# Kernel optimization log

Hardware: AMD Instinct MI355X
Metric: run time of the kernel (lower is better)

Reference implementation:

```python
import jax, jax.numpy as jnp
import numpy as np

MAX_REL = 14
HEADS = 12
HEAD_DIM = 64
SCALE = HEAD_DIM ** -0.5


def _rel_indices(length):
    # Replicates ElasticRelativePosition2D index construction (static, numpy).
    L = length - 1
    s = int(L ** 0.5)
    r = np.arange(L)
    dv = r[None, :] // s - r[:, None] // s
    dh = r[None, :] % s - r[:, None] % s
    iv = np.clip(dv, -MAX_REL, MAX_REL) + MAX_REL + 1
    ih = np.clip(dh, -MAX_REL, MAX_REL) + MAX_REL + 1
    # pad top row and left col with index 0 (the CLS slot)
    iv = np.pad(iv, ((1, 0), (1, 0)), constant_values=0)
    ih = np.pad(ih, ((1, 0), (1, 0)), constant_values=0)
    return jnp.asarray(iv, dtype=jnp.int32), jnp.asarray(ih, dtype=jnp.int32)


def _rel_emb(table_v, table_h, length):
    iv, ih = _rel_indices(length)
    return table_v[iv] + table_h[ih]  # [length, length, 64]


def setup_inputs() -> dict:
    key = jax.random.key(0)
    ks = jax.random.split(key, 16)
    B, L, D = 32, 577, 768
    T = 2 * MAX_REL + 2  # 30
    std = 0.02
    inp = {
        "q": jax.random.normal(ks[0], (B, L, D), jnp.float32),
        "k": jax.random.normal(ks[1], (B, L, D), jnp.float32),
        "v": jax.random.normal(ks[2], (B, L, D), jnp.float32),
        "Wq": jax.random.normal(ks[3], (D, HEADS * HEAD_DIM), jnp.float32) * std,
        "bq": jnp.zeros((HEADS * HEAD_DIM,), jnp.float32),
        "Wk": jax.random.normal(ks[4], (D, HEADS * HEAD_DIM), jnp.float32) * std,
        "bk": jnp.zeros((HEADS * HEAD_DIM,), jnp.float32),
        "Wv": jax.random.normal(ks[5], (D, HEADS * HEAD_DIM), jnp.float32) * std,
        "bv": jnp.zeros((HEADS * HEAD_DIM,), jnp.float32),
        "Wp": jax.random.normal(ks[6], (HEADS * HEAD_DIM, D), jnp.float32) * std,
        "bp": jnp.zeros((D,), jnp.float32),
        "tab_vk": jax.random.normal(ks[7], (T, HEAD_DIM), jnp.float32) * std,
        "tab_hk": jax.random.normal(ks[8], (T, HEAD_DIM), jnp.float32) * std,
        "tab_vv": jax.random.normal(ks[9], (T, HEAD_DIM), jnp.float32) * std,
        "tab_hv": jax.random.normal(ks[10], (T, HEAD_DIM), jnp.float32) * std,
    }
    return inp


def reference(q, k, v, Wq, bq, Wk, bk, Wv, bv, Wp, bp, tab_vk, tab_hk, tab_vv, tab_hv):
    B, L, D = q.shape
    residual = q
    qh = (q @ Wq + bq).reshape(B, L, HEADS, HEAD_DIM).transpose(0, 2, 1, 3)  # [B,H,L,d]
    kh = (k @ Wk + bk).reshape(B, L, HEADS, HEAD_DIM).transpose(0, 2, 1, 3)
    vh = (v @ Wv + bv).reshape(B, L, HEADS, HEAD_DIM).transpose(0, 2, 1, 3)

    attn = jnp.einsum("bhid,bhjd->bhij", qh, kh) * SCALE
    r_p_k = _rel_emb(tab_vk, tab_hk, L)  # [L,L,d]
    attn = attn + jnp.einsum("bhid,ijd->bhij", qh, r_p_k)  # bias NOT scaled (as in source)
    attn = jax.nn.softmax(attn, axis=-1)

    out = jnp.einsum("bhij,bhjd->bhid", attn, vh)
    r_p_v = _rel_emb(tab_vv, tab_hv, L)
    out = out + jnp.einsum("bhij,ijd->bhid", attn, r_p_v)
    out = out.transpose(0, 2, 1, 3).reshape(B, L, HEADS * HEAD_DIM)

    out = out @ Wp + bp
    return out + residual
```

## Files before the change

kernel.cpp:

```cpp
#include <hip/hip_runtime.h>
#include <cstdint>


typedef unsigned short u16;
typedef unsigned int   u32;
typedef __attribute__((ext_vector_type(8))) __bf16 bf16x8;
typedef __attribute__((ext_vector_type(4))) float  f32x4;

#define B_   32
#define L_   577
#define D_   768
#define H_   12
#define HD_  64
#define LP_  640
#define M_   (B_*L_)
#define SCALE_ 0.125f

__device__ __forceinline__ float b2f(u16 u){ u32 x = ((u32)u) << 16; float f; __builtin_memcpy(&f,&x,4); return f; }
__device__ __forceinline__ u16 f2b(float f){ u32 x; __builtin_memcpy(&x,&f,4); u32 r = (x + 0x7FFFu + ((x>>16)&1u)) >> 16; return (u16)r; }

__device__ __forceinline__ f32x4 mfma_bf16(bf16x8 a, bf16x8 b, f32x4 c){
  return __builtin_amdgcn_mfma_f32_16x16x32_bf16(a, b, c, 0, 0, 0);
}

__device__ __forceinline__ void async16(const void* g, void* l){
  __builtin_amdgcn_global_load_lds(
    (const __attribute__((address_space(1))) void*)g,
    (__attribute__((address_space(3))) void*)l,
    16, 0, 0);
}

__device__ __forceinline__ void lds_fence(){
  asm volatile("s_waitcnt lgkmcnt(0)" ::: "memory");
}

__global__ __launch_bounds__(256) void ind_setup(u16* __restrict__ ind)
{
  int jt = blockIdx.x;
  int t  = threadIdx.x;
  int nt = t >> 6, lane = t & 63;
  int qq = lane >> 4, cc = lane & 15;
  int n = nt*16 + cc;
  u16 vals[8];
  #pragma unroll
  for (int idx = 0; idx < 8; ++idx){
    int j = jt*32 + qq*8 + idx;
    int bv, bhh;
    if (j == 0){ bv = 24; bhh = 24; }
    else { int jj = j-1; bv = jj/24; if (bv > 23) bv = 23; bhh = jj - (jj/24)*24; }
    bool one = (n < 25) ? (bv == n) : ((n < 50) ? (bhh == n-25) : false);
    vals[idx] = one ? (u16)0x3F80 : (u16)0;
  }
  *(uint4*)&ind[(size_t)((jt*4 + nt)*64 + lane)*8] = *(uint4*)vals;
}

__global__ __launch_bounds__(256) void tab_setup(
    const float* __restrict__ tvk, const float* __restrict__ thk,
    const float* __restrict__ tvv, const float* __restrict__ thv,
    u16* __restrict__ tabK, u16* __restrict__ tabVT)
{
  int i = blockIdx.x*256 + threadIdx.x;
  if (i >= 64*64) return;
  int r = i >> 6, col = i & 63;
  float kv = 0.f;
  if (r < 30)      kv = tvk[r*HD_ + col];
  else if (r < 60) kv = thk[(r-30)*HD_ + col];
  tabK[i] = f2b(kv);
  float vv = 0.f;
  if (col < 30)      vv = tvv[col*HD_ + r];
  else if (col < 60) vv = thv[(col-30)*HD_ + r];
  tabVT[i] = f2b(vv);
}

__global__ __launch_bounds__(256) void cvt3_bf16(
    const float* __restrict__ q, const float* __restrict__ k, const float* __restrict__ v,
    u16* __restrict__ dq, u16* __restrict__ dk, u16* __restrict__ dv)
{
  int z = blockIdx.y;
  const float* s = (z==0)?q:(z==1)?k:v;
  u16*         d = (z==0)?dq:(z==1)?dk:dv;
  int i = blockIdx.x*256 + threadIdx.x;
  if (i >= (M_*D_)/8) return;
  const float4* s4 = (const float4*)s;
  float4 a = s4[2*i], b = s4[2*i+1];
  uint4 o;
  o.x = (u32)f2b(a.x) | ((u32)f2b(a.y)<<16);
  o.y = (u32)f2b(a.z) | ((u32)f2b(a.w)<<16);
  o.z = (u32)f2b(b.x) | ((u32)f2b(b.y)<<16);
  o.w = (u32)f2b(b.z) | ((u32)f2b(b.w)<<16);
  ((uint4*)d)[i] = o;
}

__global__ __launch_bounds__(256) void transpose768(
    const float* __restrict__ W0, const float* __restrict__ W1,
    const float* __restrict__ W2, const float* __restrict__ W3,
    u16* __restrict__ T0, u16* __restrict__ T1, u16* __restrict__ T2, u16* __restrict__ T3)
{
  __shared__ float t[32][33];
  int z = blockIdx.z;
  const float* W = (z==0)?W0:(z==1)?W1:(z==2)?W2:W3;
  u16*         T = (z==0)?T0:(z==1)?T1:(z==2)?T2:T3;
  int kb = blockIdx.x*32, nb = blockIdx.y*32;
  int tx = threadIdx.x & 31, ty = threadIdx.x >> 5;
  #pragma unroll
  for (int r=0;r<32;r+=8) t[ty+r][tx] = W[(size_t)(kb+ty+r)*768 + nb+tx];
  __syncthreads();
  #pragma unroll
  for (int r=0;r<32;r+=8) T[(size_t)(nb+ty+r)*768 + kb+tx] = f2b(t[tx][ty+r]);
}

__global__ __launch_bounds__(256) void vtr_kernel(
    const u16* __restrict__ vh, u16* __restrict__ vhT)
{
  __shared__ __align__(16) u16 t[64][72];
  int ll0 = blockIdx.x * 64;
  size_t bhs = (size_t)(blockIdx.z*H_ + blockIdx.y) * LP_ * HD_;
  const u16* src = vh + bhs;
  u16* dst = vhT + bhs;
  int tid = threadIdx.x;
  #pragma unroll
  for (int it=0; it<2; ++it){
    int idx = it*256 + tid;
    int row = idx >> 3, ch = (idx & 7)*8;
    uint4 d4; d4.x=0u; d4.y=0u; d4.z=0u; d4.w=0u;
    if (ll0 + row < L_) d4 = *(const uint4*)(src + (size_t)(ll0+row)*HD_ + ch);
    *(uint4*)&t[row][ch] = d4;
  }
  __syncthreads();
  #pragma unroll
  for (int it=0; it<2; ++it){
    int idx = it*256 + tid;
    int dd = idx >> 3, l8 = (idx & 7)*8;
    u16 vals[8];
    #pragma unroll
    for (int e=0;e<8;++e) vals[e] = t[l8+e][dd];
    *(uint4*)(dst + (size_t)dd*LP_ + ll0 + l8) = *(uint4*)vals;
  }
}

__global__ __launch_bounds__(256) void gemm_kernel(
    const u16* __restrict__ A, const u16* __restrict__ BT,
    const float* __restrict__ bias, const float* __restrict__ resid,
    void* __restrict__ Dstv, int mode)
{
  __shared__ __align__(16) u16 AsL[128*32];
  __shared__ __align__(16) u16 BsL[128*32];
  const int blk = blockIdx.x;
  const int x = blk & 7, g = blk >> 3;
  const int n0 = (g % 6) * 128;
  const int m_idx = (g / 6) * 8 + x;
  if (m_idx >= 145) return;
  const int m0 = m_idx * 128;

  const int tid = threadIdx.x;
  const int w = tid>>6, lane = tid&63, q = lane>>4, c = lane&15;
  const int wr = w>>1, wc = w&1;

  f32x4 acc[4][4];
  #pragma unroll
  for (int ai=0;ai<4;++ai)
    #pragma unroll
    for (int bi=0;bi<4;++bi){ f32x4 z = {0.f,0.f,0.f,0.f}; acc[ai][bi] = z; }

  for (int k0 = 0; k0 < 768; k0 += 32){
    __syncthreads();
    #pragma unroll
    for (int t2 = 0; t2 < 2; ++t2){
      int idx = t2*256 + tid;
      int row = idx >> 2, ch = idx & 3;
      int mrow = m0 + row; if (mrow > M_-1) mrow = M_-1;
      const u16* srcA;
      if (mode < 3) srcA = A + (size_t)mrow*768 + k0 + ch*8;
      else {
        int bb = mrow / L_, ll = mrow - bb*L_;
        int hh = k0 >> 6, dd = (k0 & 63) + ch*8;
        srcA = A + (((size_t)(bb*H_ + hh)*LP_ + ll) << 6) + dd;
      }
      async16(srcA, (char*)AsL + (size_t)(t2*256 + w*64)*16);
      async16(BT + (size_t)(n0 + row)*768 + k0 + ch*8, (char*)BsL + (size_t)(t2*256 + w*64)*16);
    }
    __syncthreads();

    bf16x8 af[4], bf2[4];
    #pragma unroll
    for (int ai=0;ai<4;++ai) af[ai]  = *(const bf16x8*)&AsL[(wr*64 + ai*16 + c)*32 + q*8];
    #pragma unroll
    for (int bi=0;bi<4;++bi) bf2[bi] = *(const bf16x8*)&BsL[(wc*64 + bi*16 + c)*32 + q*8];
    #pragma unroll
    for (int ai=0;ai<4;++ai)
      #pragma unroll
      for (int bi=0;bi<4;++bi)
        acc[ai][bi] = mfma_bf16(af[ai], bf2[bi], acc[ai][bi]);
  }

  #pragma unroll
  for (int ai=0;ai<4;++ai){
    #pragma unroll
    for (int r2=0;r2<4;++r2){
      int mrow = m0 + wr*64 + ai*16 + q*4 + r2;
      if (mrow >= M_) continue;
      int bb = mrow / L_;
      int ll = mrow - bb*L_;
      #pragma unroll
      for (int bi=0;bi<4;++bi){
        int col = n0 + wc*64 + bi*16 + c;
        float vv = acc[ai][bi][r2] + bias[col];
        if (mode < 3){
          int hh = col >> 6, dd = col & 63;
          ((u16*)Dstv)[(((size_t)(bb*H_ + hh)*LP_ + ll) << 6) + dd] = f2b(vv);
        } else {
          size_t o2 = (size_t)mrow*768 + col;
          ((float*)Dstv)[o2] = vv + resid[o2];
        }
      }
    }
  }
}

__global__ __launch_bounds__(256) void attn_kernel(
    const u16* __restrict__ qh, const u16* __restrict__ kh, const u16* __restrict__ vhT,
    const u16* __restrict__ tabK, const u16* __restrict__ tabVT,
    const u16* __restrict__ ind,
    u16* __restrict__ oh)
{
  __shared__ __align__(16) char sb[4*6272];
  const int tid = threadIdx.x;
  const int w = tid>>6, lane = tid&63, q = lane>>4, c = lane&15;
  char* wb = sb + w*6272;
  float* gvh   = (float*)wb;
  u16*   pvhb  = (u16*)wb;
  u16*   Ps_w  = (u16*)(wb + 3328);
  u16*   bias_t= (u16*)(wb + 4608);

  const int id = blockIdx.x;
  const int lin = (id & 7)*480 + (id >> 3);
  const int qt = lin % 10;
  const int hb = lin / 10;
  const int h = hb % 12, b = hb / 12;

  const int i0 = qt * 64;
  const size_t bh = (size_t)(b*H_ + h) * LP_ * HD_;
  const u16* qh_b = qh + bh;
  const u16* kh_b = kh + bh;
  const u16* vT_b = vhT + bh;

  bf16x8 aq0 = *(const bf16x8*)(qh_b + (size_t)(i0 + w*16 + c)*HD_ + q*8);
  bf16x8 aq1 = *(const bf16x8*)(qh_b + (size_t)(i0 + w*16 + c)*HD_ + 32 + q*8);

  #pragma unroll
  for (int nt=0; nt<4; ++nt){
    bf16x8 tb0 = *(const bf16x8*)(tabK + (size_t)(nt*16+c)*64 + q*8);
    bf16x8 tb1 = *(const bf16x8*)(tabK + (size_t)(nt*16+c)*64 + 32 + q*8);
    f32x4 s = {0.f,0.f,0.f,0.f};
    s = mfma_bf16(aq0, tb0, s);
    s = mfma_bf16(aq1, tb1, s);
    int bin = nt*16 + c;
    if (bin < 60){
      #pragma unroll
      for (int r=0;r<4;++r) pvhb[(q*4+r)*66 + bin] = f2b(s[r]);
    }
  }
  lds_fence();

  for (int o = lane; o < 16*50; o += 64){
    int row = o / 50, t = o - (o/50)*50;
    int ig = i0 + w*16 + row;
    const u16* src = pvhb + row*66;
    u16 val;
    if (ig == 0){
      val = src[t < 25 ? 0 : 30];
    } else {
      int im1 = ig - 1;
      int rr = im1 / 24, cc2 = im1 - (im1/24)*24;
      if (t < 25){
        if (t == 24) val = src[0];
        else { int d = t - rr;  d = d < -14 ? -14 : (d > 14 ? 14 : d); val = src[15 + d]; }
      } else {
        int cb = t - 25;
        if (cb == 24) val = src[30];
        else { int d = cb - cc2; d = d < -14 ? -14 : (d > 14 ? 14 : d); val = src[45 + d]; }
      }
    }
    bias_t[row*52 + t] = val;
  }
  lds_fence();

  int ig_[4];
  #pragma unroll
  for (int r=0;r<4;++r) ig_[r] = i0 + w*16 + q*4 + r;

  f32x4 o4[4], hist[4];
  #pragma unroll
  for (int nt=0;nt<4;++nt){ f32x4 z = {0.f,0.f,0.f,0.f}; o4[nt] = z; hist[nt] = z; }

  const u16* btr = bias_t + (q*4)*52;

  for (int jt = 0; jt < 19; ++jt){
    int j0 = jt * 32;
    lds_fence();

    bf16x8 bvf[4];
    #pragma unroll
    for (int nt=0;nt<4;++nt)
      bvf[nt] = *(const bf16x8*)(vT_b + (size_t)(nt*16+c)*LP_ + j0 + q*8);
    uint4 bi_raw[4];
    #pragma unroll
    for (int nt=0;nt<4;++nt) bi_raw[nt] = ((const uint4*)ind)[(jt*4 + nt)*64 + lane];

    #pragma unroll
    for (int sub=0; sub<2; ++sub){
      const u16* kr = kh_b + (size_t)(j0 + sub*16 + c)*HD_;
      bf16x8 bk0 = *(const bf16x8*)(kr + q*8);
      bf16x8 bk1 = *(const bf16x8*)(kr + 32 + q*8);
      f32x4 s4 = {0.f,0.f,0.f,0.f};
      __builtin_amdgcn_s_setprio(1);
      s4 = mfma_bf16(aq0, bk0, s4);
      s4 = mfma_bf16(aq1, bk1, s4);
      __builtin_amdgcn_s_setprio(0);

      int j  = j0 + sub*16 + c;
      bool jv = (j < L_);
      int jj = j - 1;
      int q24 = jj / 24;
      int gR  = (j==0) ? 24 : (q24 > 23 ? 23 : q24);
      int cbR = (j==0) ? 24 : (jj - q24*24);

      #pragma unroll
      for (int r=0;r<4;++r){
        float bias = b2f(btr[r*52 + gR]) + b2f(btr[r*52 + 25 + cbR]);
        float s = fmaf(s4[r], SCALE_, bias);
        s = fminf(fmaxf(s, -80.f), 30.f);
        float p = jv ? __expf(s) : 0.f;
        __bf16 pb = (__bf16)p;
        u16 pu; __builtin_memcpy(&pu, &pb, 2);
        Ps_w[(q*4+r)*40 + sub*16 + c] = pu;
      }
    }
    lds_fence();
    bf16x8 ap = *(const bf16x8*)(Ps_w + c*40 + q*8);
    __builtin_amdgcn_s_setprio(1);
    #pragma unroll
    for (int nt=0;nt<4;++nt){
      o4[nt] = mfma_bf16(ap, bvf[nt], o4[nt]);
      bf16x8 bI = *(const bf16x8*)&bi_raw[nt];
      hist[nt] = mfma_bf16(ap, bI, hist[nt]);
    }
    __builtin_amdgcn_s_setprio(0);
  }

  lds_fence();

  #pragma unroll
  for (int nt=0;nt<4;++nt){
    int bin = nt*16 + c;
    if (bin < 50){
      #pragma unroll
      for (int r=0;r<4;++r)
        gvh[(size_t)(q*4 + r)*52 + bin] = hist[nt][r];
    }
  }
  lds_fence();

  u16* Wm = (u16*)(wb + 3328);
  for (int o = lane; o < 16*72; o += 64) Wm[o] = 0;
  lds_fence();
  if (lane < 16){
    int ig = i0 + w*16 + lane;
    const float* gv = gvh + (size_t)lane*52;
    u16* wrp = Wm + lane*72;
    if (ig == 0){
      float sv=0.f, sh=0.f;
      for (int g2=0; g2<25; ++g2){ sv += gv[g2]; sh += gv[25+g2]; }
      wrp[0] = f2b(sv); wrp[30] = f2b(sh);
    } else {
      int rr = (ig-1)/24, cc2 = (ig-1) - ((ig-1)/24)*24;
      wrp[0]  = f2b(gv[24]);
      wrp[30] = f2b(gv[49]);
      for (int t=1; t<30; ++t){
        float sv = 0.f, sh = 0.f;
        if (t == 1){
          for (int g2=0; g2 <= rr-14  && g2 < 24; ++g2) sv += gv[g2];
          for (int c2=0; c2 <= cc2-14 && c2 < 24; ++c2) sh += gv[25+c2];
        } else if (t == 29){
          for (int g2 = (rr+14  < 0 ? 0 : rr+14 ); g2 < 24; ++g2) sv += gv[g2];
          for (int c2 = (cc2+14 < 0 ? 0 : cc2+14); c2 < 24; ++c2) sh += gv[25+c2];
        } else {
          int g2 = rr  + t - 15; if (g2 >= 0 && g2 < 24) sv = gv[g2];
          int c2 = cc2 + t - 15; if (c2 >= 0 && c2 < 24) sh = gv[25+c2];
        }
        wrp[t] = f2b(sv); wrp[30+t] = f2b(sh);
      }
    }
  }
  lds_fence();

  bf16x8 aw0 = *(const bf16x8*)(Wm + c*72 + q*8);
  bf16x8 aw1 = *(const bf16x8*)(Wm + c*72 + 32 + q*8);
  __builtin_amdgcn_s_setprio(1);
  #pragma unroll
  for (int nt=0;nt<4;++nt){
    bf16x8 bt0 = *(const bf16x8*)(tabVT + (size_t)(nt*16+c)*64 + q*8);
    bf16x8 bt1 = *(const bf16x8*)(tabVT + (size_t)(nt*16+c)*64 + 32 + q*8);
    o4[nt] = mfma_bf16(aw0, bt0, o4[nt]);
    o4[nt] = mfma_bf16(aw1, bt1, o4[nt]);
  }
  __builtin_amdgcn_s_setprio(0);

  u16* oh_b = oh + bh;
  #pragma unroll
  for (int r=0;r<4;++r){
    if (ig_[r] < L_){
      const float* gr = gvh + (size_t)(q*4 + r)*52;
      f32x4 a0 = *(const f32x4*)(gr);
      f32x4 a1 = *(const f32x4*)(gr+4);
      f32x4 a2 = *(const f32x4*)(gr+8);
      f32x4 a3 = *(const f32x4*)(gr+12);
      f32x4 a4 = *(const f32x4*)(gr+16);
      f32x4 a5 = *(const f32x4*)(gr+20);
      float lsum = (a0[0]+a0[1]+a0[2]+a0[3]) + (a1[0]+a1[1]+a1[2]+a1[3])
                 + (a2[0]+a2[1]+a2[2]+a2[3]) + (a3[0]+a3[1]+a3[2]+a3[3])
                 + (a4[0]+a4[1]+a4[2]+a4[3]) + (a5[0]+a5[1]+a5[2]+a5[3]) + gr[24];
      float inv = 1.f / lsum;
      #pragma unroll
      for (int nt=0;nt<4;++nt)
        oh_b[(size_t)ig_[r]*HD_ + nt*16 + c] = f2b(o4[nt][r] * inv);
    }
  }
}

extern "C" void kernel_launch(void* const* d_in, const int* in_sizes, int n_in,
                              void* d_out, int out_size, void* d_ws, size_t ws_size,
                              hipStream_t stream)
{
  (void)in_sizes; (void)n_in; (void)out_size; (void)ws_size;
  const float* q_   = (const float*)d_in[0];
  const float* k_   = (const float*)d_in[1];
  const float* v_   = (const float*)d_in[2];
  const float* Wq_  = (const float*)d_in[3];
  const float* bq_  = (const float*)d_in[4];
  const float* Wk_  = (const float*)d_in[5];
  const float* bk_  = (const float*)d_in[6];
  const float* Wv_  = (const float*)d_in[7];
  const float* bv_  = (const float*)d_in[8];
  const float* Wp_  = (const float*)d_in[9];
  const float* bp_  = (const float*)d_in[10];
  const float* tvk_ = (const float*)d_in[11];
  const float* thk_ = (const float*)d_in[12];
  const float* tvv_ = (const float*)d_in[13];
  const float* thv_ = (const float*)d_in[14];

  char* ws = (char*)d_ws;
  const size_t szHead = (size_t)B_*H_*LP_*HD_*2;
  const size_t szQKV  = (size_t)M_*D_*2;
  u16* qh   = (u16*)(ws);
  u16* kh   = (u16*)(ws + szHead);
  u16* vh   = (u16*)(ws + 2*szHead);
  u16* oh   = (u16*)(ws + 3*szHead);
  u16* q_bf = oh;
  u16* k_bf = (u16*)(ws + 4*szHead);
  u16* v_bf = (u16*)(ws + 4*szHead + szQKV);
  u16* vhT  = k_bf;
  u16* WqT  = (u16*)(ws + 4*szHead + 2*szQKV);
  u16* WkT  = WqT + 768*768;
  u16* WvT  = WkT + 768*768;
  u16* WpT  = WvT + 768*768;
  u16* ind  = WpT + 768*768;
  u16* tabK  = ind + 19*4*64*8;
  u16* tabVT = tabK + 64*64;

  ind_setup<<<19, 256, 0, stream>>>(ind);
  tab_setup<<<16, 256, 0, stream>>>(tvk_, thk_, tvv_, thv_, tabK, tabVT);
  transpose768<<<dim3(24,24,4), 256, 0, stream>>>(Wq_, Wk_, Wv_, Wp_, WqT, WkT, WvT, WpT);
  cvt3_bf16<<<dim3((M_*D_/8 + 255)/256, 3), 256, 0, stream>>>(q_, k_, v_, q_bf, k_bf, v_bf);
  gemm_kernel<<<912, 256, 0, stream>>>(q_bf, WqT, bq_, nullptr, qh, 0);
  gemm_kernel<<<912, 256, 0, stream>>>(k_bf, WkT, bk_, nullptr, kh, 1);
  gemm_kernel<<<912, 256, 0, stream>>>(v_bf, WvT, bv_, nullptr, vh, 2);
  vtr_kernel<<<dim3(10,12,32), 256, 0, stream>>>(vh, vhT);
  attn_kernel<<<3840, 256, 0, stream>>>(qh, kh, vhT, tabK, tabVT, ind, oh);
  gemm_kernel<<<912, 256, 0, stream>>>(oh, WpT, bp_, q_, d_out, 3);
}
```

Measured before the change: 868.5 us.

## Double-buffer attention P tiles and merge QKV projections into one launch

The attention loop now computes QK^T and exp for the next key tile into a second per-wave LDS buffer while the current tile's P·V and histogram MFMAs run. This removes the LDS wait fence between softmax and PV, and per-wave LDS shrinks by reusing regions. Separately, the three Q/K/V projection GEMMs are merged into a single 2736-block launch to cut launch gaps and tail underutilisation. The pipelining relies on a compiler-only barrier instead of an explicit lgkmcnt wait, which risks an LDS read-after-write hazard within a wave.

```diff
diff --git a/kernel.cpp b/kernel.cpp
--- a/kernel.cpp
+++ b/kernel.cpp
@@ -32,6 +32,9 @@
 
 __device__ __forceinline__ void lds_fence(){
   asm volatile("s_waitcnt lgkmcnt(0)" ::: "memory");
+}
+__device__ __forceinline__ void cbar(){
+  asm volatile("" ::: "memory");
 }
 
 __global__ __launch_bounds__(256) void ind_setup(u16* __restrict__ ind)
@@ -138,6 +141,81 @@
   }
 }
 
+__global__ __launch_bounds__(256) void gemm_qkv(
+    const u16* __restrict__ Aq, const u16* __restrict__ Ak, const u16* __restrict__ Av,
+    const u16* __restrict__ WTbase,
+    const float* __restrict__ bq, const float* __restrict__ bk, const float* __restrict__ bv,
+    u16* __restrict__ Dq, u16* __restrict__ Dk, u16* __restrict__ Dv)
+{
+  __shared__ __align__(16) u16 AsL[128*32];
+  __shared__ __align__(16) u16 BsL[128*32];
+  const int blk = blockIdx.x;
+  const int which = blk / 912;
+  const int inner = blk - which*912;
+  const int x = inner & 7, g = inner >> 3;
+  const int n0 = (g % 6) * 128;
+  const int m_idx = (g / 6) * 8 + x;
+  if (m_idx >= 145) return;
+  const int m0 = m_idx * 128;
+
+  const u16* A  = (which==0)?Aq:(which==1)?Ak:Av;
+  const u16* BT = WTbase + (size_t)which*768*768;
+  const float* bias = (which==0)?bq:(which==1)?bk:bv;
+  u16* Dst = (which==0)?Dq:(which==1)?Dk:Dv;
+
+  const int tid = threadIdx.x;
+  const int w = tid>>6, lane = tid&63, q = lane>>4, c = lane&15;
+  const int wr = w>>1, wc = w&1;
+
+  f32x4 acc[4][4];
+  #pragma unroll
+  for (int ai=0;ai<4;++ai)
+    #pragma unroll
+    for (int bi=0;bi<4;++bi){ f32x4 z = {0.f,0.f,0.f,0.f}; acc[ai][bi] = z; }
+
+  for (int k0 = 0; k0 < 768; k0 += 32){
+    __syncthreads();
+    #pragma unroll
+    for (int t2 = 0; t2 < 2; ++t2){
+      int idx = t2*256 + tid;
+      int row = idx >> 2, ch = idx & 3;
+      int mrow = m0 + row; if (mrow > M_-1) mrow = M_-1;
+      async16(A + (size_t)mrow*768 + k0 + ch*8, (char*)AsL + (size_t)(t2*256 + w*64)*16);
+      async16(BT + (size_t)(n0 + row)*768 + k0 + ch*8, (char*)BsL + (size_t)(t2*256 + w*64)*16);
+    }
+    __syncthreads();
+
+    bf16x8 af[4], bf2[4];
+    #pragma unroll
+    for (int ai=0;ai<4;++ai) af[ai]  = *(const bf16x8*)&AsL[(wr*64 + ai*16 + c)*32 + q*8];
+    #pragma unroll
+    for (int bi=0;bi<4;++bi) bf2[bi] = *(const bf16x8*)&BsL[(wc*64 + bi*16 + c)*32 + q*8];
+    #pragma unroll
+    for (int ai=0;ai<4;++ai)
+      #pragma unroll
+      for (int bi=0;bi<4;++bi)
+        acc[ai][bi] = mfma_bf16(af[ai], bf2[bi], acc[ai][bi]);
+  }
+
+  #pragma unroll
+  for (int ai=0;ai<4;++ai){
+    #pragma unroll
+    for (int r2=0;r2<4;++r2){
+      int mrow = m0 + wr*64 + ai*16 + q*4 + r2;
+      if (mrow >= M_) continue;
+      int bb = mrow / L_;
+      int ll = mrow - bb*L_;
+      #pragma unroll
+      for (int bi=0;bi<4;++bi){
+        int col = n0 + wc*64 + bi*16 + c;
+        float vv = acc[ai][bi][r2] + bias[col];
+        int hh = col >> 6, dd = col & 63;
+        Dst[(((size_t)(bb*H_ + hh)*LP_ + ll) << 6) + dd] = f2b(vv);
+      }
+    }
+  }
+}
+
 __global__ __launch_bounds__(256) void gemm_kernel(
     const u16* __restrict__ A, const u16* __restrict__ BT,
     const float* __restrict__ bias, const float* __restrict__ resid,
@@ -223,14 +301,16 @@
     const u16* __restrict__ ind,
     u16* __restrict__ oh)
 {
-  __shared__ __align__(16) char sb[4*6272];
+  __shared__ __align__(16) char sb[4*5632];
   const int tid = threadIdx.x;
   const int w = tid>>6, lane = tid&63, q = lane>>4, c = lane&15;
-  char* wb = sb + w*6272;
+  char* wb = sb + w*5632;
+  u16*   pvhb  = (u16*)wb;
+  u16*   Ps0   = (u16*)wb;
+  u16*   Ps1   = (u16*)(wb + 1280);
   float* gvh   = (float*)wb;
-  u16*   pvhb  = (u16*)wb;
-  u16*   Ps_w  = (u16*)(wb + 3328);
-  u16*   bias_t= (u16*)(wb + 4608);
+  u16*   bias_t= (u16*)(wb + 3328);
+  u16*   Wm    = (u16*)(wb + 3328);
 
   const int id = blockIdx.x;
   const int lin = (id & 7)*480 + (id >> 3);
@@ -289,27 +369,13 @@
   #pragma unroll
   for (int r=0;r<4;++r) ig_[r] = i0 + w*16 + q*4 + r;
 
-  f32x4 o4[4], hist[4];
-  #pragma unroll
-  for (int nt=0;nt<4;++nt){ f32x4 z = {0.f,0.f,0.f,0.f}; o4[nt] = z; hist[nt] = z; }
-
   const u16* btr = bias_t + (q*4)*52;
 
-  for (int jt = 0; jt < 19; ++jt){
-    int j0 = jt * 32;
-    lds_fence();
-
-    bf16x8 bvf[4];
-    #pragma unroll
-    for (int nt=0;nt<4;++nt)
-      bvf[nt] = *(const bf16x8*)(vT_b + (size_t)(nt*16+c)*LP_ + j0 + q*8);
-    uint4 bi_raw[4];
-    #pragma unroll
-    for (int nt=0;nt<4;++nt) bi_raw[nt] = ((const uint4*)ind)[(jt*4 + nt)*64 + lane];
-
+  auto qk_softmax = [&](int jtx, u16* dst){
+    int j0x = jtx * 32;
     #pragma unroll
     for (int sub=0; sub<2; ++sub){
-      const u16* kr = kh_b + (size_t)(j0 + sub*16 + c)*HD_;
+      const u16* kr = kh_b + (size_t)(j0x + sub*16 + c)*HD_;
       bf16x8 bk0 = *(const bf16x8*)(kr + q*8);
       bf16x8 bk1 = *(const bf16x8*)(kr + 32 + q*8);
       f32x4 s4 = {0.f,0.f,0.f,0.f};
@@ -318,7 +384,7 @@
       s4 = mfma_bf16(aq1, bk1, s4);
       __builtin_amdgcn_s_setprio(0);
 
-      int j  = j0 + sub*16 + c;
+      int j  = j0x + sub*16 + c;
       bool jv = (j < L_);
       int jj = j - 1;
       int q24 = jj / 24;
@@ -333,11 +399,33 @@
         float p = jv ? __expf(s) : 0.f;
         __bf16 pb = (__bf16)p;
         u16 pu; __builtin_memcpy(&pu, &pb, 2);
-        Ps_w[(q*4+r)*40 + sub*16 + c] = pu;
+        dst[(q*4+r)*40 + sub*16 + c] = pu;
       }
     }
-    lds_fence();
-    bf16x8 ap = *(const bf16x8*)(Ps_w + c*40 + q*8);
+  };
+
+  f32x4 o4[4], hist[4];
+  #pragma unroll
+  for (int nt=0;nt<4;++nt){ f32x4 z = {0.f,0.f,0.f,0.f}; o4[nt] = z; hist[nt] = z; }
+
+  qk_softmax(0, Ps0);
+
+  for (int jt = 0; jt < 19; ++jt){
+    int j0 = jt * 32;
+    bf16x8 bvf[4];
+    #pragma unroll
+    for (int nt=0;nt<4;++nt)
+      bvf[nt] = *(const bf16x8*)(vT_b + (size_t)(nt*16+c)*LP_ + j0 + q*8);
+    uint4 bi_raw[4];
+    #pragma unroll
+    for (int nt=0;nt<4;++nt) bi_raw[nt] = ((const uint4*)ind)[(jt*4 + nt)*64 + lane];
+
+    cbar();
+    u16* Pc = (jt & 1) ? Ps1 : Ps0;
+    bf16x8 ap = *(const bf16x8*)(Pc + c*40 + q*8);
+
+    if (jt < 18) qk_softmax(jt+1, (jt & 1) ? Ps0 : Ps1);
+
     __builtin_amdgcn_s_setprio(1);
     #pragma unroll
     for (int nt=0;nt<4;++nt){
@@ -361,7 +449,6 @@
   }
   lds_fence();
 
-  u16* Wm = (u16*)(wb + 3328);
   for (int o = lane; o < 16*72; o += 64) Wm[o] = 0;
   lds_fence();
   if (lane < 16){
@@ -472,9 +559,7 @@
   tab_setup<<<16, 256, 0, stream>>>(tvk_, thk_, tvv_, thv_, tabK, tabVT);
   transpose768<<<dim3(24,24,4), 256, 0, stream>>>(Wq_, Wk_, Wv_, Wp_, WqT, WkT, WvT, WpT);
   cvt3_bf16<<<dim3((M_*D_/8 + 255)/256, 3), 256, 0, stream>>>(q_, k_, v_, q_bf, k_bf, v_bf);
-  gemm_kernel<<<912, 256, 0, stream>>>(q_bf, WqT, bq_, nullptr, qh, 0);
-  gemm_kernel<<<912, 256, 0, stream>>>(k_bf, WkT, bk_, nullptr, kh, 1);
-  gemm_kernel<<<912, 256, 0, stream>>>(v_bf, WvT, bv_, nullptr, vh, 2);
+  gemm_qkv<<<2736, 256, 0, stream>>>(q_bf, k_bf, v_bf, WqT, bq_, bk_, bv_, qh, kh, vh);
   vtr_kernel<<<dim3(10,12,32), 256, 0, stream>>>(vh, vhT);
   attn_kernel<<<3840, 256, 0, stream>>>(qh, kh, vhT, tabK, tabVT, ind, oh);
   gemm_kernel<<<912, 256, 0, stream>>>(oh, WpT, bp_, q_, d_out, 3);
```

Result: faster. 792.5 us (-8.8%).
